# Optimization experiments

Hardware: AMD Instinct MI355X
Metric: run time of the kernel (lower is better)

Reference implementation:

```python
import jax, jax.numpy as jnp
import numpy as np

N_HEADS = 16
EPS = 1e-6  # WanSelfAttention passes eps=1e-6 to WanRMSNorm
ROPE_MAX = 1024


def _rmsnorm(v, g):
    # WanRMSNorm: normalize in fp32 over the full `dim`, then scale by weight
    v32 = v.astype(jnp.float32)
    n = v32 * jax.lax.rsqrt(jnp.mean(v32 * v32, axis=-1, keepdims=True) + EPS)
    return n * g


def _rope(x, f, h, w, fc, fs):
    # x: [b, s, n, d] with s == f*h*w. Complex rope: (a+bi) * (cos + i sin)
    b, s, n, d = x.shape
    c = d // 2
    c1 = c - 2 * (c // 3)
    c2 = c // 3

    def build(t):  # t: [ROPE_MAX, c] -> [1, s, 1, c]
        tf, th, tw = t[:, :c1], t[:, c1:c1 + c2], t[:, c1 + c2:]
        pf = jnp.broadcast_to(tf[:f, None, None, :], (f, h, w, c1))
        ph = jnp.broadcast_to(th[None, :h, None, :], (f, h, w, c2))
        pw = jnp.broadcast_to(tw[None, None, :w, :], (f, h, w, c2))
        return jnp.concatenate([pf, ph, pw], axis=-1).reshape(1, f * h * w, 1, c)

    cosv, sinv = build(fc), build(fs)
    xr = x.astype(jnp.float32).reshape(b, s, n, c, 2)
    a, bi = xr[..., 0], xr[..., 1]
    out_r = a * cosv - bi * sinv
    out_i = a * sinv + bi * cosv
    return jnp.stack([out_r, out_i], axis=-1).reshape(b, s, n, d)


def setup_inputs() -> dict:
    key = jax.random.key(0)
    ks = jax.random.split(key, 12)
    b, s, dim = 1, 2048, 2048
    n, d = N_HEADS, 2048 // N_HEADS  # d = 128, c = 64
    f, h, w = 2, 32, 32              # f*h*w == s
    c = d // 2
    c1 = c - 2 * (c // 3)
    c2 = c // 3

    # Realistic rope tables per band (cos/sin of pos * inv_freq)
    pos = np.arange(ROPE_MAX, dtype=np.float64)[:, None]
    ang = []
    for cx in (c1, c2, c2):
        inv = 1.0 / (10000.0 ** (np.arange(cx, dtype=np.float64) / cx))
        ang.append(pos * inv[None, :])
    ang = np.concatenate(ang, axis=1)
    freqs_cos = jnp.asarray(np.cos(ang), dtype=jnp.float32)
    freqs_sin = jnp.asarray(np.sin(ang), dtype=jnp.float32)

    scale = 1.0 / np.sqrt(dim)
    inp = {
        "x": jax.random.normal(ks[0], (b, s, dim), dtype=jnp.float32),
        "freqs_cos": freqs_cos,
        "freqs_sin": freqs_sin,
        "Wq": jax.random.normal(ks[1], (dim, dim), dtype=jnp.float32) * scale,
        "bq": jnp.zeros((dim,), dtype=jnp.float32),
        "Wk": jax.random.normal(ks[2], (dim, dim), dtype=jnp.float32) * scale,
        "bk": jnp.zeros((dim,), dtype=jnp.float32),
        "Wv": jax.random.normal(ks[3], (dim, dim), dtype=jnp.float32) * scale,
        "bv": jnp.zeros((dim,), dtype=jnp.float32),
        "Wo": jax.random.normal(ks[4], (dim, dim), dtype=jnp.float32) * scale,
        "bo": jnp.zeros((dim,), dtype=jnp.float32),
        "gq": jnp.ones((dim,), dtype=jnp.float32),
        "gk": jnp.ones((dim,), dtype=jnp.float32),
        "seq_lens": jnp.array([s], dtype=jnp.int32),
        "f": f,
        "h": h,
        "w": w,
    }
    return inp


def reference(x, freqs_cos, freqs_sin, Wq, bq, Wk, bk, Wv, bv, Wo, bo, gq, gk,
              seq_lens, f, h, w):
    b, s, dim = x.shape
    n = N_HEADS
    d = dim // n

    q = _rmsnorm(x @ Wq.T + bq, gq).reshape(b, s, n, d)
    k = _rmsnorm(x @ Wk.T + bk, gk).reshape(b, s, n, d)
    v = (x @ Wv.T + bv).reshape(b, s, n, d)

    q = _rope(q, f, h, w, freqs_cos, freqs_sin)
    k = _rope(k, f, h, w, freqs_cos, freqs_sin)

    scale = np.float32(1.0 / np.sqrt(d))
    scores = jnp.einsum('bqnd,bknd->bnqk', q, k) * scale  # [b,n,s,s]
    key_mask = jnp.arange(s)[None, :] < seq_lens[:, None]  # [b,s] (k_lens)
    scores = jnp.where(key_mask[:, None, None, :], scores, -jnp.inf)
    probs = jax.nn.softmax(scores, axis=-1)
    out = jnp.einsum('bnqk,bknd->bqnd', probs, v).reshape(b, s, dim)
    return out @ Wo.T + bo
```

## Files before the change

### kernel.cpp

```cpp
#include <hip/hip_runtime.h>
#include <cstdint>
#include <cmath>

typedef unsigned int uint;
typedef unsigned short ushort;
typedef __bf16 bf16_t;
typedef bf16_t bf16x8 __attribute__((ext_vector_type(8)));
typedef float f32x4 __attribute__((ext_vector_type(4)));
typedef float f32x16 __attribute__((ext_vector_type(16)));

#define LOG2E 1.44269504088896340736f

__device__ __forceinline__ ushort f2bf(float f) {
  uint x = __float_as_uint(f);
  x += 0x7fffu + ((x >> 16) & 1u);
  return (ushort)(x >> 16);
}
__device__ __forceinline__ uint pack2(float lo, float hi) {
  return (uint)f2bf(lo) | ((uint)f2bf(hi) << 16);
}
__device__ __forceinline__ uint cvt_pk_bf16(float lo, float hi) {
  uint r;
  asm("v_cvt_pk_bf16_f32 %0, %1, %2" : "=v"(r) : "v"(lo), "v"(hi));
  return r;
}

__device__ __forceinline__ void gload_lds16(const void* gsrc, void* ldsdst) {
  typedef const __attribute__((address_space(1))) unsigned int* gp_t;
  typedef __attribute__((address_space(3))) unsigned int* lp_t;
  __builtin_amdgcn_global_load_lds((gp_t)(uintptr_t)gsrc,
                                   (lp_t)(unsigned int)(uintptr_t)ldsdst,
                                   16, 0, 0);
}

__global__ __launch_bounds__(256) void cvt5(const float* __restrict__ x,
                                            const float* __restrict__ wq,
                                            const float* __restrict__ wk,
                                            const float* __restrict__ wv,
                                            const float* __restrict__ wo,
                                            ushort* __restrict__ xb,
                                            ushort* __restrict__ wqkv,
                                            ushort* __restrict__ wob,
                                            int nx8, int nw8) {
  const int y = blockIdx.y;
  const float* src;
  ushort* dst;
  int n8;
  if (y == 0)      { src = x;  dst = xb;  n8 = nx8; }
  else if (y == 4) { src = wo; dst = wob; n8 = nw8; }
  else {
    src = (y == 1) ? wq : (y == 2) ? wk : wv;
    dst = wqkv + (size_t)(y - 1) * nw8 * 8;
    n8 = nw8;
  }
  int i = blockIdx.x * blockDim.x + threadIdx.x;
  if (i >= n8) return;
  const float4* s4 = (const float4*)src;
  float4 a = s4[i * 2], b = s4[i * 2 + 1];
  uint4 o;
  o.x = pack2(a.x, a.y); o.y = pack2(a.z, a.w);
  o.z = pack2(b.x, b.y); o.w = pack2(b.z, b.w);
  ((uint4*)dst)[i] = o;
}

__global__ __launch_bounds__(512) void gemm_qkv192(const ushort* __restrict__ A,
                                                   const ushort* __restrict__ B,
                                                   const float* __restrict__ bq,
                                                   const float* __restrict__ bk,
                                                   const float* __restrict__ bv,
                                                   float* __restrict__ qpre,
                                                   float* __restrict__ kpre,
                                                   ushort* __restrict__ Vt,
                                                   int K, int S_) {
  __shared__ __align__(16) unsigned char ldsA[65536];
  __shared__ __align__(16) unsigned char ldsB[49152];
  const int t = threadIdx.x, l = t & 63;
  const int w = t >> 6;
  const int g = l >> 4, c = l & 15;
  const int wr = w >> 2, wc = w & 3;
  const int tm = blockIdx.y * 256, tn = blockIdx.x * 192;

  const int srow = t >> 3;
  const int schunk = (t & 7) ^ (srow & 7);
  const ushort* Ag = A + (size_t)(tm + srow) * K + schunk * 8;
  const ushort* Bg = B + (size_t)(tn + srow) * K + schunk * 8;
  const size_t rK64 = (size_t)64 * K;

#define STG_A(kt, u) gload_lds16(Ag + (size_t)(u) * rK64 + ((kt) << 6),   \
    ldsA + ((kt)&1) * 32768 + (u) * 8192 + t * 16)
#define STG_B(kt, u) gload_lds16(Bg + (size_t)(u) * rK64 + ((kt) << 6),   \
    ldsB + ((kt)&1) * 24576 + (u) * 8192 + t * 16)

  f32x4 acc[8][3] = {};
  bf16x8 af[2][2], bfr[3][2];
  const int cr = c * 128;
  const int sw0 = ((0 * 4 + g) ^ (c & 7)) << 4;
  const int sw1 = ((1 * 4 + g) ^ (c & 7)) << 4;

#define RDA(d, q) do {                                                               \
    _Pragma("unroll") for (int mm = 0; mm < 2; ++mm) {                               \
      const unsigned char* p_ = ldsA + (d)*32768 + (wr*128 + (q)*32 + mm*16)*128 + cr; \
      af[mm][0] = *(const bf16x8*)(p_ + sw0);                                        \
      af[mm][1] = *(const bf16x8*)(p_ + sw1); }                                      \
  } while (0)
#define RDB(d) do {                                                                 \
    _Pragma("unroll") for (int nn = 0; nn < 3; ++nn) {                              \
      const unsigned char* p_ = ldsB + (d)*24576 + (wc*48 + nn*16)*128 + cr;        \
      bfr[nn][0] = *(const bf16x8*)(p_ + sw0);                                      \
      bfr[nn][1] = *(const bf16x8*)(p_ + sw1); }                                    \
  } while (0)
#define MM(q) do {                                                                  \
    __builtin_amdgcn_s_setprio(1);                                                  \
    _Pragma("unroll") for (int mm = 0; mm < 2; ++mm)                                \
    _Pragma("unroll") for (int nn = 0; nn < 3; ++nn) {                              \
      acc[(q)*2+mm][nn] = __builtin_amdgcn_mfma_f32_16x16x32_bf16(                  \
          af[mm][0], bfr[nn][0], acc[(q)*2+mm][nn], 0, 0, 0);                       \
      acc[(q)*2+mm][nn] = __builtin_amdgcn_mfma_f32_16x16x32_bf16(                  \
          af[mm][1], bfr[nn][1], acc[(q)*2+mm][nn], 0, 0, 0); }                     \
    __builtin_amdgcn_s_setprio(0);                                                  \
  } while (0)
#define BAR() __builtin_amdgcn_s_barrier()

  STG_B(0, 0); STG_B(0, 1); STG_B(0, 2);
  STG_A(0, 0); STG_A(0, 1); STG_A(0, 2); STG_A(0, 3);
  STG_B(1, 0); STG_B(1, 1); STG_B(1, 2);
  STG_A(1, 0); STG_A(1, 1); STG_A(1, 2);
  asm volatile("s_waitcnt vmcnt(6)" ::: "memory");
  BAR();

  const int NITER = K >> 7;
  for (int i = 0; i < NITER; ++i) {
    const int k1 = 2 * i + 1, k2 = 2 * i + 2, k3 = 2 * i + 3;
    const bool st = (i + 1 < NITER);
    RDA(0, 0); RDB(0);
    STG_A(k1, 3);
    MM(0); BAR();
    RDA(0, 1);
    if (st) { STG_B(k2, 0); STG_B(k2, 1); }
    MM(1); BAR();
    RDA(0, 2);
    if (st) { STG_B(k2, 2); STG_A(k2, 0); }
    MM(2); BAR();
    RDA(0, 3);
    if (st) { STG_A(k2, 1); STG_A(k2, 2); }
    MM(3);
    if (st) asm volatile("s_waitcnt vmcnt(6)" ::: "memory");
    else    asm volatile("s_waitcnt vmcnt(0)" ::: "memory");
    BAR();
    RDA(1, 0); RDB(1);
    if (st) STG_A(k2, 3);
    MM(0); BAR();
    RDA(1, 1);
    if (st) { STG_B(k3, 0); STG_B(k3, 1); }
    MM(1); BAR();
    RDA(1, 2);
    if (st) { STG_B(k3, 2); STG_A(k3, 0); }
    MM(2); BAR();
    RDA(1, 3);
    if (st) { STG_A(k3, 1); STG_A(k3, 2); }
    MM(3);
    if (st) asm volatile("s_waitcnt vmcnt(6)" ::: "memory");
    else    asm volatile("s_waitcnt vmcnt(0)" ::: "memory");
    BAR();
  }

#undef STG_A
#undef STG_B
#undef RDA
#undef RDB
#undef MM
#undef BAR

#pragma unroll
  for (int n = 0; n < 3; ++n) {
    int col = tn + wc * 48 + n * 16 + c;
    int sel = col >> 11;
    if (sel < 2) {
      float* outp = sel ? kpre : qpre;
      const float* bias = sel ? bk : bq;
      int col2 = col & 2047;
      float bvv = bias[col2];
#pragma unroll
      for (int m = 0; m < 8; ++m) {
        int row0 = tm + wr * 128 + m * 16 + g * 4;
#pragma unroll
        for (int i = 0; i < 4; ++i)
          outp[(size_t)(row0 + i) * 2048 + col2] = acc[m][n][i] + bvv;
      }
    } else {
      int colv = col - 4096;
      float bvv = bv[colv];
#pragma unroll
      for (int m = 0; m < 8; ++m) {
        int row0 = tm + wr * 128 + m * 16 + g * 4;
        uint2 o;
        o.x = pack2(acc[m][n][0] + bvv, acc[m][n][1] + bvv);
        o.y = pack2(acc[m][n][2] + bvv, acc[m][n][3] + bvv);
        *(uint2*)(Vt + (size_t)colv * S_ + row0) = o;
      }
    }
  }
}

__global__ __launch_bounds__(512) void gemm_wo_db(const ushort* __restrict__ A,
                                                  const ushort* __restrict__ B,
                                                  float* __restrict__ pbuf, int K) {
  __shared__ __align__(16) unsigned char As[16384];
  __shared__ __align__(16) unsigned char Bs[16384];
  const int t = threadIdx.x, l = t & 63, w = t >> 6;
  const int g = l >> 4, c = l & 15;
  const int wr = w >> 1, wc = w & 1;
  const int tm = blockIdx.y * 128, tn = blockIdx.x * 128;
  const int ks = blockIdx.z;
  const int k0 = ks * (K >> 1);

  const int srow = w * 16 + (l >> 2);
  const int schunk = (l & 3) ^ (srow & 3);
  const ushort* Ag = A + (size_t)(tm + srow) * K + k0 + schunk * 8;
  const ushort* Bg = B + (size_t)(tn + srow) * K + k0 + schunk * 8;

  f32x4 acc[2][4] = {};

  const int NT = K >> 6;
  gload_lds16(Ag, As + w * 1024);
  gload_lds16(Bg, Bs + w * 1024);

  for (int j = 0; j < NT; ++j) {
    const int buf = j & 1, nb = buf ^ 1;
    if (j + 1 < NT) {
      const int kt1 = (j + 1) << 5;
      gload_lds16(Ag + kt1, As + nb * 8192 + w * 1024);
      gload_lds16(Bg + kt1, Bs + nb * 8192 + w * 1024);
      asm volatile("s_waitcnt vmcnt(2)" ::: "memory");
    } else {
      asm volatile("s_waitcnt vmcnt(0)" ::: "memory");
    }
    __builtin_amdgcn_s_barrier();

    const unsigned char* Ab = As + buf * 8192;
    const unsigned char* Bb = Bs + buf * 8192;
    bf16x8 af[2], bfr[4];
#pragma unroll
    for (int m = 0; m < 2; ++m) {
      int row = wr * 32 + m * 16 + c;
      af[m] = *(const bf16x8*)(Ab + row * 64 + ((g ^ (row & 3)) << 4));
    }
#pragma unroll
    for (int n = 0; n < 4; ++n) {
      int row = wc * 64 + n * 16 + c;
      bfr[n] = *(const bf16x8*)(Bb + row * 64 + ((g ^ (row & 3)) << 4));
    }
#pragma unroll
    for (int m = 0; m < 2; ++m)
#pragma unroll
      for (int n = 0; n < 4; ++n)
        acc[m][n] = __builtin_amdgcn_mfma_f32_16x16x32_bf16(af[m], bfr[n], acc[m][n], 0, 0, 0);

    __builtin_amdgcn_s_barrier();
  }

  float* out = pbuf + (size_t)ks * 2048 * 2048;
#pragma unroll
  for (int n = 0; n < 4; ++n) {
    int col = tn + wc * 64 + n * 16 + c;
#pragma unroll
    for (int m = 0; m < 2; ++m) {
      int row0 = tm + wr * 32 + m * 16 + g * 4;
#pragma unroll
      for (int i = 0; i < 4; ++i)
        out[(size_t)(row0 + i) * 2048 + col] = acc[m][n][i];
    }
  }
}

__global__ __launch_bounds__(256) void reduce_wo(const float* __restrict__ p,
                                                 const float* __restrict__ bo,
                                                 float* __restrict__ out, int n4) {
  int i = blockIdx.x * blockDim.x + threadIdx.x;
  if (i >= n4) return;
  float4 a = ((const float4*)p)[i];
  float4 b = ((const float4*)p)[i + n4];
  float4 bb = *(const float4*)(bo + ((i * 4) & 2047));
  float4 o;
  o.x = a.x + b.x + bb.x; o.y = a.y + b.y + bb.y;
  o.z = a.z + b.z + bb.z; o.w = a.w + b.w + bb.w;
  ((float4*)out)[i] = o;
}

__global__ __launch_bounds__(256) void fuse_rms_rope(const float* __restrict__ qpre,
                                                     const float* __restrict__ kpre,
                                                     const float* __restrict__ gq,
                                                     const float* __restrict__ gk,
                                                     const float* __restrict__ fc,
                                                     const float* __restrict__ fs,
                                                     const int* __restrict__ pH,
                                                     const int* __restrict__ pW,
                                                     ushort* __restrict__ Qb,
                                                     ushort* __restrict__ Kb,
                                                     int dim, float foldq) {
  const int which = blockIdx.y;
  const float* pre = which ? kpre : qpre;
  const float* gw = which ? gk : gq;
  ushort* outp = which ? Kb : Qb;
  const float fold = which ? 1.0f : foldq;

  const int p = blockIdx.x, t = threadIdx.x;
  const float* row = pre + (size_t)p * dim;
  float v[8];
  {
    float4 a = *(const float4*)(row + t * 8);
    float4 b = *(const float4*)(row + t * 8 + 4);
    v[0] = a.x; v[1] = a.y; v[2] = a.z; v[3] = a.w;
    v[4] = b.x; v[5] = b.y; v[6] = b.z; v[7] = b.w;
  }
  float ss = 0.f;
#pragma unroll
  for (int i = 0; i < 8; ++i) ss += v[i] * v[i];
#pragma unroll
  for (int off = 32; off; off >>= 1) ss += __shfl_xor(ss, off);
  __shared__ float wsum[4];
  if ((t & 63) == 0) wsum[t >> 6] = ss;
  __syncthreads();
  float rstd = rsqrtf((wsum[0] + wsum[1] + wsum[2] + wsum[3]) * (1.0f / dim) + 1e-6f);
  float gv[8];
  {
    float4 a = *(const float4*)(gw + t * 8);
    float4 b = *(const float4*)(gw + t * 8 + 4);
    gv[0] = a.x; gv[1] = a.y; gv[2] = a.z; gv[3] = a.w;
    gv[4] = b.x; gv[5] = b.y; gv[6] = b.z; gv[7] = b.w;
  }
#pragma unroll
  for (int i = 0; i < 8; ++i) v[i] = v[i] * rstd * gv[i];

  const int H = pH[0], W = pW[0];
  const int hw = H * W;
  const int fr = p / hw;
  const int rem = p - fr * hw;
  const int hh = rem / W;
  const int ww = rem - hh * W;
  const int hd = dim / 16;
  const int cd = hd >> 1;
  const int c2 = cd / 3, c1 = cd - 2 * c2;
  const int j0 = ((t * 8) % hd) >> 1;

  uint ob[4];
#pragma unroll
  for (int q = 0; q < 4; ++q) {
    int j = j0 + q;
    int ri = (j < c1) ? fr : ((j < c1 + c2) ? hh : ww);
    float cs = fc[ri * cd + j];
    float sn = fs[ri * cd + j];
    float a = v[2 * q], b = v[2 * q + 1];
    ob[q] = pack2((a * cs - b * sn) * fold, (a * sn + b * cs) * fold);
  }
  uint4 o4; o4.x = ob[0]; o4.y = ob[1]; o4.z = ob[2]; o4.w = ob[3];
  *(uint4*)(outp + (size_t)p * dim + t * 8) = o4;
}

__global__ __launch_bounds__(512, 2) void attn32(const ushort* __restrict__ Qb,
                                                 const ushort* __restrict__ Kb,
                                                 const ushort* __restrict__ Vt,
                                                 ushort* __restrict__ Ob,
                                                 const int* __restrict__ seq_lens,
                                                 int S_, int DIMc) {
  __shared__ __align__(16) unsigned char smem[66560];
  float* mlbuf = (float*)(smem + 65536);
  const int t = threadIdx.x, l = t & 63, w = t >> 6;
  const int qsub = w & 3, ksp = w >> 2;
  const int h = l >> 5, ql = l & 31;

  const int orig = blockIdx.y * gridDim.x + blockIdx.x;
  const int nwg = gridDim.x * gridDim.y;
  const int lin = (orig & 7) * (nwg >> 3) + (orig >> 3);
  const int q0 = (lin % gridDim.x) * 128;
  const int head = lin / gridDim.x;
  const int kvlen = seq_lens[0];

  unsigned char* sk_s = smem + ksp * 16384;
  unsigned char* sv_s = smem + 32768 + ksp * 16384;

  bf16x8 qf[8];
  {
    const ushort* qp = Qb + (size_t)(q0 + qsub * 32 + ql) * DIMc + head * 128 + h * 8;
#pragma unroll
    for (int s = 0; s < 8; ++s) qf[s] = *(const bf16x8*)(qp + s * 16);
  }

  f32x16 ofr[4] = {};
  float m_run = -1e30f, l_run = 0.f;

  const int nt = (kvlen + 63) >> 6;
  const int half = (nt + 1) >> 1;
  const int tbase = ksp ? half : 0;
  const int mycnt = ksp ? (nt - half) : half;

#define MKK(IT, KO, KD) size_t KO; uint KD;                                     \
  { int kr_ = qsub * 16 + (IT) * 4 + (l >> 4); int kc_ = (l & 15) ^ (kr_ & 15); \
    KO = (size_t)kr_ * DIMc + head * 128 + kc_ * 8;                             \
    KD = (uint)(ksp * 16384 + qsub * 4096 + (IT) * 1024 + l * 16); }
#define MKV(IT, VO, VD) size_t VO; uint VD;                                     \
  { int vr_ = qsub * 32 + (IT) * 8 + (l >> 3); int vc_ = (l & 7) ^ (vr_ & 7);   \
    VO = (size_t)(head * 128 + vr_) * S_ + vc_ * 8;                             \
    VD = (uint)(32768 + ksp * 16384 + qsub * 4096 + (IT) * 1024 + l * 16); }
  MKK(0, kO0, kD0) MKK(1, kO1, kD1) MKK(2, kO2, kD2) MKK(3, kO3, kD3)
  MKV(0, vO0, vD0) MKV(1, vO1, vD1) MKV(2, vO2, vD2) MKV(3, vO3, vD3)
#undef MKK
#undef MKV

  uint4 rk0, rk1, rk2, rk3, rv0, rv1, rv2, rv3;
  if (mycnt > 0) {
    const size_t kbq = (size_t)(tbase * 64) * DIMc;
    const int vq = tbase * 64;
    rk0 = *(const uint4*)(Kb + kO0 + kbq);
    rk1 = *(const uint4*)(Kb + kO1 + kbq);
    rk2 = *(const uint4*)(Kb + kO2 + kbq);
    rk3 = *(const uint4*)(Kb + kO3 + kbq);
    rv0 = *(const uint4*)(Vt + vO0 + vq);
    rv1 = *(const uint4*)(Vt + vO1 + vq);
    rv2 = *(const uint4*)(Vt + vO2 + vq);
    rv3 = *(const uint4*)(Vt + vO3 + vq);
  }

  for (int tt = 0; tt < half; ++tt) {
    __builtin_amdgcn_s_barrier();
    if (tt < mycnt) {
      *(uint4*)(smem + kD0) = rk0; *(uint4*)(smem + kD1) = rk1;
      *(uint4*)(smem + kD2) = rk2; *(uint4*)(smem + kD3) = rk3;
      *(uint4*)(smem + vD0) = rv0; *(uint4*)(smem + vD1) = rv1;
      *(uint4*)(smem + vD2) = rv2; *(uint4*)(smem + vD3) = rv3;
      if (tt + 1 < mycnt) {
        const size_t kbq = (size_t)((tbase + tt + 1) * 64) * DIMc;
        const int vq = (tbase + tt + 1) * 64;
        rk0 = *(const uint4*)(Kb + kO0 + kbq);
        rk1 = *(const uint4*)(Kb + kO1 + kbq);
        rk2 = *(const uint4*)(Kb + kO2 + kbq);
        rk3 = *(const uint4*)(Kb + kO3 + kbq);
        rv0 = *(const uint4*)(Vt + vO0 + vq);
        rv1 = *(const uint4*)(Vt + vO1 + vq);
        rv2 = *(const uint4*)(Vt + vO2 + vq);
        rv3 = *(const uint4*)(Vt + vO3 + vq);
      }
    }
    asm volatile("s_waitcnt lgkmcnt(0)" ::: "memory");
    __builtin_amdgcn_s_barrier();
    __builtin_amdgcn_sched_barrier(0);
    if (tt >= mycnt) continue;
    const int kv0 = (tbase + tt) * 64;

    f32x16 sfr[2] = {};
    __builtin_amdgcn_s_setprio(1);
#pragma unroll
    for (int kb = 0; kb < 2; ++kb) {
      const unsigned char* kbp = sk_s + (kb * 32 + ql) * 256;
      const int rx = (kb * 32 + ql) & 15;
#pragma unroll
      for (int s = 0; s < 8; ++s) {
        bf16x8 kf = *(const bf16x8*)(kbp + (((s * 2 + h) ^ rx) << 4));
        sfr[kb] = __builtin_amdgcn_mfma_f32_32x32x16_bf16(kf, qf[s], sfr[kb], 0, 0, 0);
      }
    }
    __builtin_amdgcn_s_setprio(0);

    if (kv0 + 64 > kvlen) {
#pragma unroll
      for (int kb = 0; kb < 2; ++kb)
#pragma unroll
        for (int r = 0; r < 16; ++r) {
          int key = kv0 + kb * 32 + (r & 3) + 8 * (r >> 2) + 4 * h;
          if (key >= kvlen) sfr[kb][r] = -1e30f;
        }
    }

    float mt = -1e30f;
#pragma unroll
    for (int kb = 0; kb < 2; ++kb)
#pragma unroll
      for (int r = 0; r < 16; ++r) mt = fmaxf(mt, sfr[kb][r]);
    mt = fmaxf(mt, __shfl_xor(mt, 32));

    if (!__all(mt <= m_run + 8.0f)) {
      float m_new = fmaxf(m_run, mt);
      float fac = __builtin_amdgcn_exp2f(m_run - m_new);
      l_run *= fac;
#pragma unroll
      for (int df = 0; df < 4; ++df) ofr[df] *= fac;
      m_run = m_new;
    }

    float ls = 0.f;
    uint u[2][4][2];
#pragma unroll
    for (int kb = 0; kb < 2; ++kb)
#pragma unroll
      for (int G = 0; G < 4; ++G) {
        float p0 = __builtin_amdgcn_exp2f(sfr[kb][G * 4 + 0] - m_run);
        float p1 = __builtin_amdgcn_exp2f(sfr[kb][G * 4 + 1] - m_run);
        float p2 = __builtin_amdgcn_exp2f(sfr[kb][G * 4 + 2] - m_run);
        float p3 = __builtin_amdgcn_exp2f(sfr[kb][G * 4 + 3] - m_run);
        ls += (p0 + p1) + (p2 + p3);
        u[kb][G][0] = cvt_pk_bf16(p0, p1);
        u[kb][G][1] = cvt_pk_bf16(p2, p3);
      }
    ls += __shfl_xor(ls, 32);
    l_run += ls;

#pragma unroll
    for (int ks = 0; ks < 4; ++ks) {
      const int kb = ks >> 1, G0 = (ks & 1) * 2;
      uint own0 = h ? u[kb][G0 + 1][0] : u[kb][G0][0];
      uint own1 = h ? u[kb][G0 + 1][1] : u[kb][G0][1];
      uint snd0 = h ? u[kb][G0][0] : u[kb][G0 + 1][0];
      uint snd1 = h ? u[kb][G0][1] : u[kb][G0 + 1][1];
      uint rcv0 = __shfl_xor(snd0, 32);
      uint rcv1 = __shfl_xor(snd1, 32);
      union { uint4 q; bf16x8 b; } uu;
      uu.q.x = h ? rcv0 : own0;
      uu.q.y = h ? rcv1 : own1;
      uu.q.z = h ? own0 : rcv0;
      uu.q.w = h ? own1 : rcv1;
      __builtin_amdgcn_s_setprio(1);
#pragma unroll
      for (int df = 0; df < 4; ++df) {
        const int row = df * 32 + ql;
        bf16x8 vf = *(const bf16x8*)(sv_s + row * 128 + (((ks * 2 + h) ^ (row & 7)) << 4));
        ofr[df] = __builtin_amdgcn_mfma_f32_32x32x16_bf16(vf, uu.b, ofr[df], 0, 0, 0);
      }
      __builtin_amdgcn_s_setprio(0);
    }
  }

  __syncthreads();
  if (ksp == 1) {
    if (h == 0) { mlbuf[qsub * 64 + ql] = m_run; mlbuf[qsub * 64 + 32 + ql] = l_run; }
    float* ob = (float*)(smem + qsub * 16384);
#pragma unroll
    for (int df = 0; df < 4; ++df)
#pragma unroll
      for (int r = 0; r < 16; ++r) {
        int d = df * 32 + (r & 3) + 8 * (r >> 2) + 4 * h;
        ob[d * 32 + ql] = ofr[df][r];
      }
  }
  __syncthreads();
  if (ksp == 0) {
    float m2 = mlbuf[qsub * 64 + ql], l2 = mlbuf[qsub * 64 + 32 + ql];
    float mstar = fmaxf(m_run, m2);
    float f1 = __builtin_amdgcn_exp2f(m_run - mstar);
    float f2 = (l2 > 0.f) ? __builtin_amdgcn_exp2f(m2 - mstar) : 0.f;
    float lstar = l_run * f1 + l2 * f2;
    float inv = 1.0f / lstar;
    float a1 = f1 * inv, a2 = f2 * inv;
    const float* ob = (const float*)(smem + qsub * 16384);
    ushort* orow = Ob + (size_t)(q0 + qsub * 32 + ql) * DIMc + head * 128;
#pragma unroll
    for (int df = 0; df < 4; ++df)
#pragma unroll
      for (int G = 0; G < 4; ++G) {
        int d0 = df * 32 + 8 * G + 4 * h;
        float v0 = ofr[df][G * 4 + 0] * a1 + ob[(d0 + 0) * 32 + ql] * a2;
        float v1 = ofr[df][G * 4 + 1] * a1 + ob[(d0 + 1) * 32 + ql] * a2;
        float v2 = ofr[df][G * 4 + 2] * a1 + ob[(d0 + 2) * 32 + ql] * a2;
        float v3 = ofr[df][G * 4 + 3] * a1 + ob[(d0 + 3) * 32 + ql] * a2;
        uint2 o; o.x = pack2(v0, v1); o.y = pack2(v2, v3);
        *(uint2*)(orow + d0) = o;
      }
  }
}

extern "C" void kernel_launch(void* const* d_in, const int* in_sizes, int n_in,
                              void* d_out, int out_size, void* d_ws, size_t ws_size,
                              hipStream_t stream) {
  const float* x  = (const float*)d_in[0];
  const float* fc = (const float*)d_in[1];
  const float* fs = (const float*)d_in[2];
  const float* Wq = (const float*)d_in[3];
  const float* bq = (const float*)d_in[4];
  const float* Wk = (const float*)d_in[5];
  const float* bk = (const float*)d_in[6];
  const float* Wv = (const float*)d_in[7];
  const float* bv = (const float*)d_in[8];
  const float* Wo = (const float*)d_in[9];
  const float* bo = (const float*)d_in[10];
  const float* gq = (const float*)d_in[11];
  const float* gk = (const float*)d_in[12];
  const int* seq  = (const int*)d_in[13];
  const int* pH   = (const int*)d_in[15];
  const int* pW   = (const int*)d_in[16];

  const int DIMc = in_sizes[4];
  const int S_   = in_sizes[0] / DIMc;

  char* ws = (char*)d_ws;
  const size_t MB = 1024ull * 1024ull;
  ushort* xb    = (ushort*)(ws + 0 * MB);
  ushort* Wqkvb = (ushort*)(ws + 8 * MB);
  ushort* Wob   = (ushort*)(ws + 32 * MB);
  float*  qpre  = (float*)(ws + 40 * MB);
  float*  kpre  = (float*)(ws + 56 * MB);
  ushort* Qb    = (ushort*)(ws + 72 * MB);
  ushort* Kb    = (ushort*)(ws + 80 * MB);
  ushort* Vt    = (ushort*)(ws + 88 * MB);
  ushort* Ob    = (ushort*)(ws + 40 * MB);
  float*  pbuf  = (float*)(ws + 56 * MB);

  const int nx8 = (S_ * DIMc) / 8;
  const int nw8 = (DIMc * DIMc) / 8;
  const int nmax = (nx8 > nw8 ? nx8 : nw8);
  cvt5<<<dim3((nmax + 255) / 256, 5), 256, 0, stream>>>(x, Wq, Wk, Wv, Wo,
                                                        xb, Wqkvb, Wob, nx8, nw8);

  gemm_qkv192<<<dim3(3 * DIMc / 192, S_ / 256), 512, 0, stream>>>(
      xb, Wqkvb, bq, bk, bv, qpre, kpre, Vt, DIMc, S_);

  const float foldq = LOG2E / sqrtf((float)(DIMc / 16));
  fuse_rms_rope<<<dim3(S_, 2), 256, 0, stream>>>(qpre, kpre, gq, gk, fc, fs, pH, pW,
                                                 Qb, Kb, DIMc, foldq);

  attn32<<<dim3(S_ / 128, 16), 512, 0, stream>>>(Qb, Kb, Vt, Ob, seq, S_, DIMc);

  gemm_wo_db<<<dim3(16, 16, 2), 512, 0, stream>>>(Ob, Wob, pbuf, DIMc);
  reduce_wo<<<(S_ * DIMc / 4 + 255) / 256, 256, 0, stream>>>(pbuf, bo, (float*)d_out,
                                                             S_ * DIMc / 4);
}
```

Before: 167.3 us.

## Replace split-K Wo GEMM and reduce with single-pass pipelined GEMM fusing bias

Measured after the change: 155.1 us (median of 2 runs). 1.08x faster.

```diff
diff --git a/kernel.cpp b/kernel.cpp
--- a/kernel.cpp
+++ b/kernel.cpp
@@ -202,89 +202,107 @@
   }
 }
 
-__global__ __launch_bounds__(512) void gemm_wo_db(const ushort* __restrict__ A,
-                                                  const ushort* __restrict__ B,
-                                                  float* __restrict__ pbuf, int K) {
-  __shared__ __align__(16) unsigned char As[16384];
-  __shared__ __align__(16) unsigned char Bs[16384];
-  const int t = threadIdx.x, l = t & 63, w = t >> 6;
+__global__ __launch_bounds__(512) void gemm_wo8p(const ushort* __restrict__ A,
+                                                 const ushort* __restrict__ B,
+                                                 const float* __restrict__ bo,
+                                                 float* __restrict__ out, int K) {
+  __shared__ __align__(16) unsigned char ldsA[32768];
+  __shared__ __align__(16) unsigned char ldsB[32768];
+  const int t = threadIdx.x, l = t & 63;
+  const int w = t >> 6;
   const int g = l >> 4, c = l & 15;
-  const int wr = w >> 1, wc = w & 1;
+  const int wr = w >> 2, wc = w & 3;
   const int tm = blockIdx.y * 128, tn = blockIdx.x * 128;
-  const int ks = blockIdx.z;
-  const int k0 = ks * (K >> 1);
-
-  const int srow = w * 16 + (l >> 2);
-  const int schunk = (l & 3) ^ (srow & 3);
-  const ushort* Ag = A + (size_t)(tm + srow) * K + k0 + schunk * 8;
-  const ushort* Bg = B + (size_t)(tn + srow) * K + k0 + schunk * 8;
-
-  f32x4 acc[2][4] = {};
-
-  const int NT = K >> 6;
-  gload_lds16(Ag, As + w * 1024);
-  gload_lds16(Bg, Bs + w * 1024);
-
-  for (int j = 0; j < NT; ++j) {
-    const int buf = j & 1, nb = buf ^ 1;
-    if (j + 1 < NT) {
-      const int kt1 = (j + 1) << 5;
-      gload_lds16(Ag + kt1, As + nb * 8192 + w * 1024);
-      gload_lds16(Bg + kt1, Bs + nb * 8192 + w * 1024);
-      asm volatile("s_waitcnt vmcnt(2)" ::: "memory");
-    } else {
-      asm volatile("s_waitcnt vmcnt(0)" ::: "memory");
+
+  const int srow = t >> 3;
+  const int schunk = (t & 7) ^ (srow & 7);
+  const ushort* Ag = A + (size_t)(tm + srow) * K + schunk * 8;
+  const ushort* Bg = B + (size_t)(tn + srow) * K + schunk * 8;
+  const size_t rK64 = (size_t)64 * K;
+
+#define WSTG_A(kt, u) gload_lds16(Ag + (size_t)(u) * rK64 + ((kt) << 6),   \
+    ldsA + ((kt)&1) * 16384 + (u) * 8192 + t * 16)
+#define WSTG_B(kt, u) gload_lds16(Bg + (size_t)(u) * rK64 + ((kt) << 6),   \
+    ldsB + ((kt)&1) * 16384 + (u) * 8192 + t * 16)
+
+  f32x4 acc[4][2] = {};
+  bf16x8 af[2][2], bfr[2][2];
+  const int cr = c * 128;
+  const int sw0 = ((0 * 4 + g) ^ (c & 7)) << 4;
+  const int sw1 = ((1 * 4 + g) ^ (c & 7)) << 4;
+
+#define WRDA(d, hf) do {                                                             \
+    _Pragma("unroll") for (int mm = 0; mm < 2; ++mm) {                               \
+      const unsigned char* p_ = ldsA + (d)*16384 + (wr*64 + ((hf)*2+mm)*16)*128 + cr; \
+      af[mm][0] = *(const bf16x8*)(p_ + sw0);                                        \
+      af[mm][1] = *(const bf16x8*)(p_ + sw1); }                                      \
+  } while (0)
+#define WRDB(d) do {                                                                \
+    _Pragma("unroll") for (int nn = 0; nn < 2; ++nn) {                              \
+      const unsigned char* p_ = ldsB + (d)*16384 + (wc*32 + nn*16)*128 + cr;        \
+      bfr[nn][0] = *(const bf16x8*)(p_ + sw0);                                      \
+      bfr[nn][1] = *(const bf16x8*)(p_ + sw1); }                                    \
+  } while (0)
+#define WMM(hf) do {                                                                \
+    __builtin_amdgcn_s_setprio(1);                                                  \
+    _Pragma("unroll") for (int mm = 0; mm < 2; ++mm)                                \
+    _Pragma("unroll") for (int nn = 0; nn < 2; ++nn) {                              \
+      acc[(hf)*2+mm][nn] = __builtin_amdgcn_mfma_f32_16x16x32_bf16(                 \
+          af[mm][0], bfr[nn][0], acc[(hf)*2+mm][nn], 0, 0, 0);                      \
+      acc[(hf)*2+mm][nn] = __builtin_amdgcn_mfma_f32_16x16x32_bf16(                 \
+          af[mm][1], bfr[nn][1], acc[(hf)*2+mm][nn], 0, 0, 0); }                    \
+    __builtin_amdgcn_s_setprio(0);                                                  \
+  } while (0)
+#define WBAR() __builtin_amdgcn_s_barrier()
+
+  WSTG_B(0, 0); WSTG_B(0, 1); WSTG_A(0, 0); WSTG_A(0, 1);
+  WSTG_B(1, 0); WSTG_B(1, 1);
+  asm volatile("s_waitcnt vmcnt(2)" ::: "memory");
+  WBAR();
+
+  const int NITER = K >> 7;
+  for (int i = 0; i < NITER; ++i) {
+    const int k1 = 2 * i + 1, k2 = 2 * i + 2, k3 = 2 * i + 3;
+    const bool st = (i + 1 < NITER);
+    WRDA(0, 0); WRDB(0);
+    WSTG_A(k1, 0); WSTG_A(k1, 1);
+    WMM(0); WBAR();
+    WRDA(0, 1);
+    if (st) { WSTG_B(k2, 0); WSTG_B(k2, 1); }
+    WMM(1);
+    if (st) asm volatile("s_waitcnt vmcnt(2)" ::: "memory");
+    else    asm volatile("s_waitcnt vmcnt(0)" ::: "memory");
+    WBAR();
+    WRDA(1, 0); WRDB(1);
+    if (st) { WSTG_A(k2, 0); WSTG_A(k2, 1); }
+    WMM(0); WBAR();
+    WRDA(1, 1);
+    if (st) { WSTG_B(k3, 0); WSTG_B(k3, 1); }
+    WMM(1);
+    if (st) asm volatile("s_waitcnt vmcnt(2)" ::: "memory");
+    else    asm volatile("s_waitcnt vmcnt(0)" ::: "memory");
+    WBAR();
+  }
+
+#undef WSTG_A
+#undef WSTG_B
+#undef WRDA
+#undef WRDB
+#undef WMM
+#undef WBAR
+
+#pragma unroll
+  for (int n = 0; n < 2; ++n) {
+    int col = tn + wc * 32 + n * 16 + c;
+    float bvv = bo[col];
+#pragma unroll
+    for (int m = 0; m < 4; ++m) {
+      int row0 = tm + wr * 64 + m * 16 + g * 4;
+#pragma unroll
+      for (int i = 0; i < 4; ++i)
+        out[(size_t)(row0 + i) * 2048 + col] = acc[m][n][i] + bvv;
     }
-    __builtin_amdgcn_s_barrier();
-
-    const unsigned char* Ab = As + buf * 8192;
-    const unsigned char* Bb = Bs + buf * 8192;
-    bf16x8 af[2], bfr[4];
-#pragma unroll
-    for (int m = 0; m < 2; ++m) {
-      int row = wr * 32 + m * 16 + c;
-      af[m] = *(const bf16x8*)(Ab + row * 64 + ((g ^ (row & 3)) << 4));
-    }
-#pragma unroll
-    for (int n = 0; n < 4; ++n) {
-      int row = wc * 64 + n * 16 + c;
-      bfr[n] = *(const bf16x8*)(Bb + row * 64 + ((g ^ (row & 3)) << 4));
-    }
-#pragma unroll
-    for (int m = 0; m < 2; ++m)
-#pragma unroll
-      for (int n = 0; n < 4; ++n)
-        acc[m][n] = __builtin_amdgcn_mfma_f32_16x16x32_bf16(af[m], bfr[n], acc[m][n], 0, 0, 0);
-
-    __builtin_amdgcn_s_barrier();
-  }
-
-  float* out = pbuf + (size_t)ks * 2048 * 2048;
-#pragma unroll
-  for (int n = 0; n < 4; ++n) {
-    int col = tn + wc * 64 + n * 16 + c;
-#pragma unroll
-    for (int m = 0; m < 2; ++m) {
-      int row0 = tm + wr * 32 + m * 16 + g * 4;
-#pragma unroll
-      for (int i = 0; i < 4; ++i)
-        out[(size_t)(row0 + i) * 2048 + col] = acc[m][n][i];
-    }
-  }
-}
-
-__global__ __launch_bounds__(256) void reduce_wo(const float* __restrict__ p,
-                                                 const float* __restrict__ bo,
-                                                 float* __restrict__ out, int n4) {
-  int i = blockIdx.x * blockDim.x + threadIdx.x;
-  if (i >= n4) return;
-  float4 a = ((const float4*)p)[i];
-  float4 b = ((const float4*)p)[i + n4];
-  float4 bb = *(const float4*)(bo + ((i * 4) & 2047));
-  float4 o;
-  o.x = a.x + b.x + bb.x; o.y = a.y + b.y + bb.y;
-  o.z = a.z + b.z + bb.z; o.w = a.w + b.w + bb.w;
-  ((float4*)out)[i] = o;
+  }
 }
 
 __global__ __launch_bounds__(256) void fuse_rms_rope(const float* __restrict__ qpre,
@@ -601,7 +619,6 @@
   ushort* Kb    = (ushort*)(ws + 80 * MB);
   ushort* Vt    = (ushort*)(ws + 88 * MB);
   ushort* Ob    = (ushort*)(ws + 40 * MB);
-  float*  pbuf  = (float*)(ws + 56 * MB);
 
   const int nx8 = (S_ * DIMc) / 8;
   const int nw8 = (DIMc * DIMc) / 8;
@@ -618,7 +635,6 @@
 
   attn32<<<dim3(S_ / 128, 16), 512, 0, stream>>>(Qb, Kb, Vt, Ob, seq, S_, DIMc);
 
-  gemm_wo_db<<<dim3(16, 16, 2), 512, 0, stream>>>(Ob, Wob, pbuf, DIMc);
-  reduce_wo<<<(S_ * DIMc / 4 + 255) / 256, 256, 0, stream>>>(pbuf, bo, (float*)d_out,
-                                                             S_ * DIMc / 4);
-}
+  gemm_wo8p<<<dim3(DIMc / 128, S_ / 128), 512, 0, stream>>>(Ob, Wob, bo,
+                                                            (float*)d_out, DIMc);
+}
```
